# Kernel tuning notes

Measured on AMD Instinct MI355X. Metric: run time of the kernel, lower is better.

Reference implementation:

```python
import jax, jax.numpy as jnp
import numpy as np

B, D, N, K = 8, 3, 65536, 64
EPS = 1e-8

def setup_inputs() -> dict:
    key = jax.random.key(0)
    k1, k2, k3 = jax.random.split(key, 3)
    return {
        "template_features": jax.random.normal(k1, (B, D, N), dtype=jnp.float32),
        "source_features": jax.random.normal(k2, (B, D, N), dtype=jnp.float32),
        "W": jax.random.normal(k3, (D, K), dtype=jnp.float32),
    }

def _gamma(features_t, W):
    # features_t: (B,N,D); logits: (B,K,N); softmax over points (dim=2, as in torch code)
    logits = jnp.einsum('bnd,dk->bkn', features_t, W)
    return jax.nn.softmax(logits, axis=2)

def _gmm_params(gamma, pts):
    # gamma: (B,K,N), pts: (B,N,D)
    n = gamma.shape[2]
    Npi = gamma.sum(axis=2) + EPS                       # (B,K)
    pi = Npi / n
    g = gamma / (Npi[:, :, None] + EPS)                 # (B,K,N)
    mu = jnp.einsum('bkn,bnd->bkd', g, pts)             # weighted mean
    # second moment; exact central form: sum_n g (x-mu)(x-mu)^T = Exx - (2 - s) mu mu^T
    Exx = jnp.einsum('bkn,bnd,bne->bkde', g, pts, pts)
    s = g.sum(axis=2)                                   # (B,K), ~1 (not exactly, due to eps)
    outer = mu[..., :, None] * mu[..., None, :]
    sigma = (Exx - (2.0 - s)[..., None, None] * outer) / (Npi[:, :, None, None] + EPS)
    return pi, mu, sigma

def _estimate_transform(mu_x, pi_x, mu_y, pi_y):
    cx = jnp.sum(mu_x * pi_x[..., None], axis=1, keepdims=True)   # (B,1,D)
    cy = jnp.sum(mu_y * pi_y[..., None], axis=1, keepdims=True)
    mu_x_c = mu_x - cx
    mu_y_c = mu_y - cy
    Wm = jnp.einsum('bkd,bke->bde', pi_x[..., None] * mu_y_c, mu_x_c)  # (B,D,D)
    U, S, Vh = jnp.linalg.svd(Wm, full_matrices=False)
    R = jnp.matmul(U, Vh)
    det = jnp.linalg.det(R)
    Vh = Vh.at[:, :, -1].multiply(jnp.sign(det)[:, None])
    R = jnp.matmul(U, Vh)
    T = cy[:, 0, :] - jnp.einsum('bde,be->bd', R, cx[:, 0, :])
    return R, T

def reference(template_features, source_features, W):
    template_pts = jnp.swapaxes(template_features, 1, 2)   # (B,N,D)
    source_pts = jnp.swapaxes(source_features, 1, 2)
    t_gamma = _gamma(template_pts, W)
    s_gamma = _gamma(source_pts, W)
    t_pi, t_mu, t_sigma = _gmm_params(t_gamma, template_pts)
    s_pi, s_mu, s_sigma = _gmm_params(s_gamma, source_pts)
    R, T = _estimate_transform(s_mu, s_pi, t_mu, t_pi)
    aligned = jnp.matmul(source_pts, jnp.swapaxes(R, 1, 2)) + T[:, None, :]
    return aligned
```

## Files before the change

kernel.cpp:

```cpp
#include <hip/hip_runtime.h>

#define N_PTS 65536
#define BATCH 8
#define KCL   64
#define CHUNK 1024
#define THREADS 256
#define LOG2E 1.44269504088896340736f

__device__ __forceinline__ double drcp(double x) {
    double r = (double)(1.0f / (float)x);
    r = r * (2.0 - x * r);
    r = r * (2.0 - x * r);
    return r;
}

__device__ __forceinline__ float hw_exp2(float x) {
    return __builtin_amdgcn_exp2f(x);
}

__global__ __launch_bounds__(THREADS) void k_sum(const float* __restrict__ tmpl,
                                                 const float* __restrict__ srcf,
                                                 const float* __restrict__ Wmat,
                                                 float* __restrict__ Zs,
                                                 float* __restrict__ Ss) {
    const int chunk = blockIdx.x;
    const int b     = blockIdx.y;
    const int set   = blockIdx.z;
    const float* feat = set ? srcf : tmpl;
    const int n0 = chunk * CHUNK;

    __shared__ float xs[3][CHUNK];
    __shared__ float red[4][KCL][4];

    const int tid = threadIdx.x;
    const float* base = feat + (size_t)b * 3 * N_PTS + n0;
    for (int i = tid; i < 3 * (CHUNK / 4); i += THREADS) {
        int d = i / (CHUNK / 4);
        int p = i % (CHUNK / 4);
        float4 v = ((const float4*)(base + (size_t)d * N_PTS))[p];
        ((float4*)&xs[d][0])[p] = v;
    }
    __syncthreads();

    const int lane = tid & 63;
    const int wv   = tid >> 6;
    const float w0 = Wmat[lane] * LOG2E;
    const float w1 = Wmat[KCL + lane] * LOG2E;
    const float w2 = Wmat[2 * KCL + lane] * LOG2E;

    float z = 0.f, s0 = 0.f, s1 = 0.f, s2 = 0.f;
    const int q0 = wv * (CHUNK / 16);
    for (int q = q0; q < q0 + CHUNK / 16; ++q) {
        float4 a = ((const float4*)&xs[0][0])[q];
        float4 c = ((const float4*)&xs[1][0])[q];
        float4 d = ((const float4*)&xs[2][0])[q];
        {
            float l = fmaf(a.x, w0, fmaf(c.x, w1, d.x * w2));
            float e = hw_exp2(l);
            z += e; s0 = fmaf(e, a.x, s0); s1 = fmaf(e, c.x, s1); s2 = fmaf(e, d.x, s2);
        }
        {
            float l = fmaf(a.y, w0, fmaf(c.y, w1, d.y * w2));
            float e = hw_exp2(l);
            z += e; s0 = fmaf(e, a.y, s0); s1 = fmaf(e, c.y, s1); s2 = fmaf(e, d.y, s2);
        }
        {
            float l = fmaf(a.z, w0, fmaf(c.z, w1, d.z * w2));
            float e = hw_exp2(l);
            z += e; s0 = fmaf(e, a.z, s0); s1 = fmaf(e, c.z, s1); s2 = fmaf(e, d.z, s2);
        }
        {
            float l = fmaf(a.w, w0, fmaf(c.w, w1, d.w * w2));
            float e = hw_exp2(l);
            z += e; s0 = fmaf(e, a.w, s0); s1 = fmaf(e, c.w, s1); s2 = fmaf(e, d.w, s2);
        }
    }
    red[wv][lane][0] = z;
    red[wv][lane][1] = s0;
    red[wv][lane][2] = s1;
    red[wv][lane][3] = s2;
    __syncthreads();
    if (tid < KCL) {
        float rz  = red[0][tid][0] + red[1][tid][0] + red[2][tid][0] + red[3][tid][0];
        float rs0 = red[0][tid][1] + red[1][tid][1] + red[2][tid][1] + red[3][tid][1];
        float rs1 = red[0][tid][2] + red[1][tid][2] + red[2][tid][2] + red[3][tid][2];
        float rs2 = red[0][tid][3] + red[1][tid][3] + red[2][tid][3] + red[3][tid][3];
        int idx = ((int)set * BATCH + b) * KCL + tid;
        atomicAdd(&Zs[idx], rz);
        atomicAdd(&Ss[idx * 3 + 0], rs0);
        atomicAdd(&Ss[idx * 3 + 1], rs1);
        atomicAdd(&Ss[idx * 3 + 2], rs2);
    }
}

__global__ void k_transform(const float* __restrict__ Zs,
                            const float* __restrict__ Ss,
                            float* __restrict__ RT) {
    const int b = threadIdx.x;
    if (b >= BATCH) return;

    const double inv_npi = 1.0 / (1.0 + 2e-8);
    const double pi_c = (1.0 + 1e-8) / (double)N_PTS;

    double Mt[3] = {0, 0, 0}, Ms[3] = {0, 0, 0};
    double P[3][3] = {{0,0,0},{0,0,0},{0,0,0}};
    for (int k = 0; k < KCL; ++k) {
        int it = (0 * BATCH + b) * KCL + k;
        int is = (1 * BATCH + b) * KCL + k;
        double izt = inv_npi * drcp((double)Zs[it]);
        double izs = inv_npi * drcp((double)Zs[is]);
        double mt[3], ms[3];
        for (int d = 0; d < 3; ++d) {
            mt[d] = (double)Ss[it * 3 + d] * izt;
            ms[d] = (double)Ss[is * 3 + d] * izs;
            Mt[d] += mt[d];
            Ms[d] += ms[d];
        }
        for (int d = 0; d < 3; ++d)
            for (int e = 0; e < 3; ++e)
                P[d][e] += mt[d] * ms[e];
    }
    double cy[3], cx[3];
    for (int d = 0; d < 3; ++d) { cy[d] = pi_c * Mt[d]; cx[d] = pi_c * Ms[d]; }

    const double coef = 2.0 * pi_c - 64.0 * pi_c * pi_c;
    double A[3][3];
    for (int d = 0; d < 3; ++d)
        for (int e = 0; e < 3; ++e)
            A[d][e] = pi_c * (P[d][e] - coef * Mt[d] * Ms[e]);

    double G[3][3];
    for (int i = 0; i < 3; ++i)
        for (int j = 0; j < 3; ++j) {
            double acc = 0;
            for (int d = 0; d < 3; ++d) acc += A[d][i] * A[d][j];
            G[i][j] = acc;
        }

    double V[3][3] = {{1,0,0},{0,1,0},{0,0,1}};
    const int pairs[3][2] = {{0,1},{0,2},{1,2}};
    const double scale0 = fabs(G[0][0]) + fabs(G[1][1]) + fabs(G[2][2]) + 1e-300;
    for (int sweep = 0; sweep < 10; ++sweep) {
        double off = fabs(G[0][1]) + fabs(G[0][2]) + fabs(G[1][2]);
        if (off < 1e-28 * scale0) break;
        for (int pi_i = 0; pi_i < 3; ++pi_i) {
            int p = pairs[pi_i][0], q = pairs[pi_i][1];
            double apq = G[p][q];
            if (fabs(apq) < 1e-30 * scale0) continue;
            double tau = (G[q][q] - G[p][p]) * drcp(2.0 * apq);
            double t = ((tau >= 0) ? 1.0 : -1.0) * drcp(fabs(tau) + sqrt(1.0 + tau * tau));
            double c = drcp(sqrt(1.0 + t * t));
            double s = t * c;
            double gpp = G[p][p], gqq = G[q][q];
            G[p][p] = gpp - t * apq;
            G[q][q] = gqq + t * apq;
            G[p][q] = G[q][p] = 0.0;
            int r = 3 - p - q;
            double grp = G[r][p], grq = G[r][q];
            G[r][p] = G[p][r] = c * grp - s * grq;
            G[r][q] = G[q][r] = s * grp + c * grq;
            for (int rr = 0; rr < 3; ++rr) {
                double vrp = V[rr][p], vrq = V[rr][q];
                V[rr][p] = c * vrp - s * vrq;
                V[rr][q] = s * vrp + c * vrq;
            }
        }
    }

    double invs[3];
    for (int i = 0; i < 3; ++i) {
        double lam = G[i][i];
        invs[i] = drcp(sqrt(lam > 1e-300 ? lam : 1e-300));
    }
    double M[3][3];
    for (int i = 0; i < 3; ++i)
        for (int j = 0; j < 3; ++j) {
            double acc = 0;
            for (int m2 = 0; m2 < 3; ++m2) acc += V[i][m2] * V[j][m2] * invs[m2];
            M[i][j] = acc;
        }
    double R0[3][3];
    for (int d = 0; d < 3; ++d)
        for (int e = 0; e < 3; ++e) {
            double acc = 0;
            for (int m2 = 0; m2 < 3; ++m2) acc += A[d][m2] * M[m2][e];
            R0[d][e] = acc;
        }

    double det = R0[0][0] * (R0[1][1] * R0[2][2] - R0[1][2] * R0[2][1])
               - R0[0][1] * (R0[1][0] * R0[2][2] - R0[1][2] * R0[2][0])
               + R0[0][2] * (R0[1][0] * R0[2][1] - R0[1][1] * R0[2][0]);
    double sg = (det >= 0.0) ? 1.0 : -1.0;
    R0[0][2] *= sg; R0[1][2] *= sg; R0[2][2] *= sg;

    double T[3];
    for (int d = 0; d < 3; ++d)
        T[d] = cy[d] - (R0[d][0] * cx[0] + R0[d][1] * cx[1] + R0[d][2] * cx[2]);

    float* rt = RT + b * 12;
    rt[0] = (float)R0[0][0]; rt[1] = (float)R0[0][1]; rt[2] = (float)R0[0][2];
    rt[3] = (float)R0[1][0]; rt[4] = (float)R0[1][1]; rt[5] = (float)R0[1][2];
    rt[6] = (float)R0[2][0]; rt[7] = (float)R0[2][1]; rt[8] = (float)R0[2][2];
    rt[9] = (float)T[0]; rt[10] = (float)T[1]; rt[11] = (float)T[2];
}

__global__ __launch_bounds__(256) void k_apply(const float* __restrict__ srcf,
                                               const float* __restrict__ RT,
                                               float* __restrict__ out) {
    const int idx = blockIdx.x * 256 + threadIdx.x;
    const int b = idx >> 16;
    const int n = idx & (N_PTS - 1);
    const float* rt = RT + b * 12;
    const float* base = srcf + (size_t)b * 3 * N_PTS;
    float x0 = base[n];
    float x1 = base[N_PTS + n];
    float x2 = base[2 * N_PTS + n];
    float y0 = fmaf(rt[0], x0, fmaf(rt[1], x1, fmaf(rt[2], x2, rt[9])));
    float y1 = fmaf(rt[3], x0, fmaf(rt[4], x1, fmaf(rt[5], x2, rt[10])));
    float y2 = fmaf(rt[6], x0, fmaf(rt[7], x1, fmaf(rt[8], x2, rt[11])));
    size_t o = (size_t)idx * 3;
    out[o + 0] = y0;
    out[o + 1] = y1;
    out[o + 2] = y2;
}

extern "C" void kernel_launch(void* const* d_in, const int* in_sizes, int n_in,
                              void* d_out, int out_size, void* d_ws, size_t ws_size,
                              hipStream_t stream) {
    const float* tmpl = (const float*)d_in[0];
    const float* srcf = (const float*)d_in[1];
    const float* Wmat = (const float*)d_in[2];
    float* out = (float*)d_out;

    float* Zs = (float*)d_ws;
    float* Ss = (float*)d_ws + 1024;
    float* RT = (float*)d_ws + 4096;

    (void)hipMemsetAsync(d_ws, 0, 4096 * sizeof(float), stream);

    dim3 grid1(N_PTS / CHUNK, BATCH, 2);
    k_sum<<<grid1, THREADS, 0, stream>>>(tmpl, srcf, Wmat, Zs, Ss);
    k_transform<<<1, 64, 0, stream>>>(Zs, Ss, RT);
    k_apply<<<(BATCH * N_PTS) / 256, 256, 0, stream>>>(srcf, RT, out);
}
```

Baseline: 111.8 us.

## Fuse transform solve into apply kernel and stream inputs directly in k_sum

k_sum no longer stages each chunk through shared memory. Each wave now reads float4 data straight from global memory over a 512-point slice, and the grid is flattened to 512 blocks. The separate single-block k_transform launch is removed. Every k_apply block now recomputes the 3x3 SVD/rotation redundantly in its first wave, using shuffle reductions across 8 lanes per batch, and keeps R/T in shared memory. k_apply also processes 4 points per thread, which cuts one launch and a serial dependency at the cost of duplicated small compute per block.

Result: faster. 100.7 us (-9.9%).

```diff
diff --git a/kernel.cpp b/kernel.cpp
--- a/kernel.cpp
+++ b/kernel.cpp
@@ -3,8 +3,6 @@
 #define N_PTS 65536
 #define BATCH 8
 #define KCL   64
-#define CHUNK 1024
-#define THREADS 256
 #define LOG2E 1.44269504088896340736f
 
 __device__ __forceinline__ double drcp(double x) {
@@ -18,42 +16,34 @@
     return __builtin_amdgcn_exp2f(x);
 }
 
-__global__ __launch_bounds__(THREADS) void k_sum(const float* __restrict__ tmpl,
-                                                 const float* __restrict__ srcf,
-                                                 const float* __restrict__ Wmat,
-                                                 float* __restrict__ Zs,
-                                                 float* __restrict__ Ss) {
-    const int chunk = blockIdx.x;
-    const int b     = blockIdx.y;
-    const int set   = blockIdx.z;
-    const float* feat = set ? srcf : tmpl;
-    const int n0 = chunk * CHUNK;
-
-    __shared__ float xs[3][CHUNK];
-    __shared__ float red[4][KCL][4];
-
-    const int tid = threadIdx.x;
-    const float* base = feat + (size_t)b * 3 * N_PTS + n0;
-    for (int i = tid; i < 3 * (CHUNK / 4); i += THREADS) {
-        int d = i / (CHUNK / 4);
-        int p = i % (CHUNK / 4);
-        float4 v = ((const float4*)(base + (size_t)d * N_PTS))[p];
-        ((float4*)&xs[d][0])[p] = v;
-    }
-    __syncthreads();
-
+__global__ __launch_bounds__(256) void k_sum(const float* __restrict__ tmpl,
+                                             const float* __restrict__ srcf,
+                                             const float* __restrict__ Wmat,
+                                             float* __restrict__ Zs,
+                                             float* __restrict__ Ss) {
+    const int tid  = threadIdx.x;
     const int lane = tid & 63;
     const int wv   = tid >> 6;
+
+    const int gw  = __builtin_amdgcn_readfirstlane(blockIdx.x * 4 + wv);
+    const int set = gw >> 10;
+    const int b   = (gw >> 7) & 7;
+    const int n0  = (gw & 127) * 512;
+    const float* bp = (set ? srcf : tmpl) + (size_t)b * 3 * N_PTS + n0;
+
     const float w0 = Wmat[lane] * LOG2E;
     const float w1 = Wmat[KCL + lane] * LOG2E;
     const float w2 = Wmat[2 * KCL + lane] * LOG2E;
 
     float z = 0.f, s0 = 0.f, s1 = 0.f, s2 = 0.f;
-    const int q0 = wv * (CHUNK / 16);
-    for (int q = q0; q < q0 + CHUNK / 16; ++q) {
-        float4 a = ((const float4*)&xs[0][0])[q];
-        float4 c = ((const float4*)&xs[1][0])[q];
-        float4 d = ((const float4*)&xs[2][0])[q];
+    const float4* p0 = (const float4*)bp;
+    const float4* p1 = (const float4*)(bp + N_PTS);
+    const float4* p2 = (const float4*)(bp + 2 * N_PTS);
+#pragma unroll 4
+    for (int q = 0; q < 128; ++q) {
+        float4 a = p0[q];
+        float4 c = p1[q];
+        float4 d = p2[q];
         {
             float l = fmaf(a.x, w0, fmaf(c.x, w1, d.x * w2));
             float e = hw_exp2(l);
@@ -75,6 +65,8 @@
             z += e; s0 = fmaf(e, a.w, s0); s1 = fmaf(e, c.w, s1); s2 = fmaf(e, d.w, s2);
         }
     }
+
+    __shared__ float red[4][KCL][4];
     red[wv][lane][0] = z;
     red[wv][lane][1] = s0;
     red[wv][lane][2] = s1;
@@ -85,7 +77,7 @@
         float rs0 = red[0][tid][1] + red[1][tid][1] + red[2][tid][1] + red[3][tid][1];
         float rs1 = red[0][tid][2] + red[1][tid][2] + red[2][tid][2] + red[3][tid][2];
         float rs2 = red[0][tid][3] + red[1][tid][3] + red[2][tid][3] + red[3][tid][3];
-        int idx = ((int)set * BATCH + b) * KCL + tid;
+        int idx = (set * BATCH + b) * KCL + tid;
         atomicAdd(&Zs[idx], rz);
         atomicAdd(&Ss[idx * 3 + 0], rs0);
         atomicAdd(&Ss[idx * 3 + 1], rs1);
@@ -93,135 +85,154 @@
     }
 }
 
-__global__ void k_transform(const float* __restrict__ Zs,
-                            const float* __restrict__ Ss,
-                            float* __restrict__ RT) {
-    const int b = threadIdx.x;
-    if (b >= BATCH) return;
-
-    const double inv_npi = 1.0 / (1.0 + 2e-8);
-    const double pi_c = (1.0 + 1e-8) / (double)N_PTS;
-
-    double Mt[3] = {0, 0, 0}, Ms[3] = {0, 0, 0};
-    double P[3][3] = {{0,0,0},{0,0,0},{0,0,0}};
-    for (int k = 0; k < KCL; ++k) {
-        int it = (0 * BATCH + b) * KCL + k;
-        int is = (1 * BATCH + b) * KCL + k;
-        double izt = inv_npi * drcp((double)Zs[it]);
-        double izs = inv_npi * drcp((double)Zs[is]);
-        double mt[3], ms[3];
-        for (int d = 0; d < 3; ++d) {
-            mt[d] = (double)Ss[it * 3 + d] * izt;
-            ms[d] = (double)Ss[is * 3 + d] * izs;
-            Mt[d] += mt[d];
-            Ms[d] += ms[d];
-        }
+__global__ __launch_bounds__(256) void k_apply(const float* __restrict__ srcf,
+                                               const float* __restrict__ Zs,
+                                               const float* __restrict__ Ss,
+                                               float* __restrict__ out) {
+    __shared__ float rt_s[BATCH][12];
+
+    if (threadIdx.x < 64) {
+        const int lane = threadIdx.x;
+        const int b    = lane >> 3;
+        const int sub  = lane & 7;
+
+        const double inv_npi = 1.0 / (1.0 + 2e-8);
+        const double pi_c = (1.0 + 1e-8) / (double)N_PTS;
+
+        double Mt[3] = {0, 0, 0}, Ms[3] = {0, 0, 0};
+        double P[3][3] = {{0,0,0},{0,0,0},{0,0,0}};
+        for (int kk = 0; kk < 8; ++kk) {
+            int k  = sub * 8 + kk;
+            int it = b * KCL + k;
+            int is = (BATCH + b) * KCL + k;
+            double izt = inv_npi * drcp((double)Zs[it]);
+            double izs = inv_npi * drcp((double)Zs[is]);
+            double mt[3], ms[3];
+            for (int d = 0; d < 3; ++d) {
+                mt[d] = (double)Ss[it * 3 + d] * izt;
+                ms[d] = (double)Ss[is * 3 + d] * izs;
+                Mt[d] += mt[d];
+                Ms[d] += ms[d];
+            }
+            for (int d = 0; d < 3; ++d)
+                for (int e = 0; e < 3; ++e)
+                    P[d][e] += mt[d] * ms[e];
+        }
+        for (int m = 1; m <= 4; m <<= 1) {
+            for (int d = 0; d < 3; ++d) {
+                Mt[d] += __shfl_xor(Mt[d], m, 64);
+                Ms[d] += __shfl_xor(Ms[d], m, 64);
+            }
+            for (int d = 0; d < 3; ++d)
+                for (int e = 0; e < 3; ++e)
+                    P[d][e] += __shfl_xor(P[d][e], m, 64);
+        }
+
+        double cy[3], cx[3];
+        for (int d = 0; d < 3; ++d) { cy[d] = pi_c * Mt[d]; cx[d] = pi_c * Ms[d]; }
+
+        const double coef = 2.0 * pi_c - 64.0 * pi_c * pi_c;
+        double A[3][3];
         for (int d = 0; d < 3; ++d)
             for (int e = 0; e < 3; ++e)
-                P[d][e] += mt[d] * ms[e];
-    }
-    double cy[3], cx[3];
-    for (int d = 0; d < 3; ++d) { cy[d] = pi_c * Mt[d]; cx[d] = pi_c * Ms[d]; }
-
-    const double coef = 2.0 * pi_c - 64.0 * pi_c * pi_c;
-    double A[3][3];
-    for (int d = 0; d < 3; ++d)
-        for (int e = 0; e < 3; ++e)
-            A[d][e] = pi_c * (P[d][e] - coef * Mt[d] * Ms[e]);
-
-    double G[3][3];
-    for (int i = 0; i < 3; ++i)
-        for (int j = 0; j < 3; ++j) {
-            double acc = 0;
-            for (int d = 0; d < 3; ++d) acc += A[d][i] * A[d][j];
-            G[i][j] = acc;
-        }
-
-    double V[3][3] = {{1,0,0},{0,1,0},{0,0,1}};
-    const int pairs[3][2] = {{0,1},{0,2},{1,2}};
-    const double scale0 = fabs(G[0][0]) + fabs(G[1][1]) + fabs(G[2][2]) + 1e-300;
-    for (int sweep = 0; sweep < 10; ++sweep) {
-        double off = fabs(G[0][1]) + fabs(G[0][2]) + fabs(G[1][2]);
-        if (off < 1e-28 * scale0) break;
-        for (int pi_i = 0; pi_i < 3; ++pi_i) {
-            int p = pairs[pi_i][0], q = pairs[pi_i][1];
-            double apq = G[p][q];
-            if (fabs(apq) < 1e-30 * scale0) continue;
-            double tau = (G[q][q] - G[p][p]) * drcp(2.0 * apq);
-            double t = ((tau >= 0) ? 1.0 : -1.0) * drcp(fabs(tau) + sqrt(1.0 + tau * tau));
-            double c = drcp(sqrt(1.0 + t * t));
-            double s = t * c;
-            double gpp = G[p][p], gqq = G[q][q];
-            G[p][p] = gpp - t * apq;
-            G[q][q] = gqq + t * apq;
-            G[p][q] = G[q][p] = 0.0;
-            int r = 3 - p - q;
-            double grp = G[r][p], grq = G[r][q];
-            G[r][p] = G[p][r] = c * grp - s * grq;
-            G[r][q] = G[q][r] = s * grp + c * grq;
-            for (int rr = 0; rr < 3; ++rr) {
-                double vrp = V[rr][p], vrq = V[rr][q];
-                V[rr][p] = c * vrp - s * vrq;
-                V[rr][q] = s * vrp + c * vrq;
-            }
-        }
-    }
-
-    double invs[3];
-    for (int i = 0; i < 3; ++i) {
-        double lam = G[i][i];
-        invs[i] = drcp(sqrt(lam > 1e-300 ? lam : 1e-300));
-    }
-    double M[3][3];
-    for (int i = 0; i < 3; ++i)
-        for (int j = 0; j < 3; ++j) {
-            double acc = 0;
-            for (int m2 = 0; m2 < 3; ++m2) acc += V[i][m2] * V[j][m2] * invs[m2];
-            M[i][j] = acc;
-        }
-    double R0[3][3];
-    for (int d = 0; d < 3; ++d)
-        for (int e = 0; e < 3; ++e) {
-            double acc = 0;
-            for (int m2 = 0; m2 < 3; ++m2) acc += A[d][m2] * M[m2][e];
-            R0[d][e] = acc;
-        }
-
-    double det = R0[0][0] * (R0[1][1] * R0[2][2] - R0[1][2] * R0[2][1])
-               - R0[0][1] * (R0[1][0] * R0[2][2] - R0[1][2] * R0[2][0])
-               + R0[0][2] * (R0[1][0] * R0[2][1] - R0[1][1] * R0[2][0]);
-    double sg = (det >= 0.0) ? 1.0 : -1.0;
-    R0[0][2] *= sg; R0[1][2] *= sg; R0[2][2] *= sg;
-
-    double T[3];
-    for (int d = 0; d < 3; ++d)
-        T[d] = cy[d] - (R0[d][0] * cx[0] + R0[d][1] * cx[1] + R0[d][2] * cx[2]);
-
-    float* rt = RT + b * 12;
-    rt[0] = (float)R0[0][0]; rt[1] = (float)R0[0][1]; rt[2] = (float)R0[0][2];
-    rt[3] = (float)R0[1][0]; rt[4] = (float)R0[1][1]; rt[5] = (float)R0[1][2];
-    rt[6] = (float)R0[2][0]; rt[7] = (float)R0[2][1]; rt[8] = (float)R0[2][2];
-    rt[9] = (float)T[0]; rt[10] = (float)T[1]; rt[11] = (float)T[2];
-}
-
-__global__ __launch_bounds__(256) void k_apply(const float* __restrict__ srcf,
-                                               const float* __restrict__ RT,
-                                               float* __restrict__ out) {
-    const int idx = blockIdx.x * 256 + threadIdx.x;
-    const int b = idx >> 16;
-    const int n = idx & (N_PTS - 1);
-    const float* rt = RT + b * 12;
-    const float* base = srcf + (size_t)b * 3 * N_PTS;
-    float x0 = base[n];
-    float x1 = base[N_PTS + n];
-    float x2 = base[2 * N_PTS + n];
-    float y0 = fmaf(rt[0], x0, fmaf(rt[1], x1, fmaf(rt[2], x2, rt[9])));
-    float y1 = fmaf(rt[3], x0, fmaf(rt[4], x1, fmaf(rt[5], x2, rt[10])));
-    float y2 = fmaf(rt[6], x0, fmaf(rt[7], x1, fmaf(rt[8], x2, rt[11])));
-    size_t o = (size_t)idx * 3;
-    out[o + 0] = y0;
-    out[o + 1] = y1;
-    out[o + 2] = y2;
+                A[d][e] = pi_c * (P[d][e] - coef * Mt[d] * Ms[e]);
+
+        double G[3][3];
+        for (int i = 0; i < 3; ++i)
+            for (int j = 0; j < 3; ++j) {
+                double acc = 0;
+                for (int d = 0; d < 3; ++d) acc += A[d][i] * A[d][j];
+                G[i][j] = acc;
+            }
+
+        double V[3][3] = {{1,0,0},{0,1,0},{0,0,1}};
+        const int pairs[3][2] = {{0,1},{0,2},{1,2}};
+        const double scale0 = fabs(G[0][0]) + fabs(G[1][1]) + fabs(G[2][2]) + 1e-300;
+        for (int sweep = 0; sweep < 10; ++sweep) {
+            double off = fabs(G[0][1]) + fabs(G[0][2]) + fabs(G[1][2]);
+            if (off < 1e-28 * scale0) break;
+            for (int pi_i = 0; pi_i < 3; ++pi_i) {
+                int p = pairs[pi_i][0], q = pairs[pi_i][1];
+                double apq = G[p][q];
+                if (fabs(apq) < 1e-30 * scale0) continue;
+                double tau = (G[q][q] - G[p][p]) * drcp(2.0 * apq);
+                double t = ((tau >= 0) ? 1.0 : -1.0) * drcp(fabs(tau) + sqrt(1.0 + tau * tau));
+                double c = drcp(sqrt(1.0 + t * t));
+                double s = t * c;
+                double gpp = G[p][p], gqq = G[q][q];
+                G[p][p] = gpp - t * apq;
+                G[q][q] = gqq + t * apq;
+                G[p][q] = G[q][p] = 0.0;
+                int r = 3 - p - q;
+                double grp = G[r][p], grq = G[r][q];
+                G[r][p] = G[p][r] = c * grp - s * grq;
+                G[r][q] = G[q][r] = s * grp + c * grq;
+                for (int rr = 0; rr < 3; ++rr) {
+                    double vrp = V[rr][p], vrq = V[rr][q];
+                    V[rr][p] = c * vrp - s * vrq;
+                    V[rr][q] = s * vrp + c * vrq;
+                }
+            }
+        }
+
+        double invs[3];
+        for (int i = 0; i < 3; ++i) {
+            double lam = G[i][i];
+            invs[i] = drcp(sqrt(lam > 1e-300 ? lam : 1e-300));
+        }
+        double M[3][3];
+        for (int i = 0; i < 3; ++i)
+            for (int j = 0; j < 3; ++j) {
+                double acc = 0;
+                for (int m2 = 0; m2 < 3; ++m2) acc += V[i][m2] * V[j][m2] * invs[m2];
+                M[i][j] = acc;
+            }
+        double R0[3][3];
+        for (int d = 0; d < 3; ++d)
+            for (int e = 0; e < 3; ++e) {
+                double acc = 0;
+                for (int m2 = 0; m2 < 3; ++m2) acc += A[d][m2] * M[m2][e];
+                R0[d][e] = acc;
+            }
+
+        double det = R0[0][0] * (R0[1][1] * R0[2][2] - R0[1][2] * R0[2][1])
+                   - R0[0][1] * (R0[1][0] * R0[2][2] - R0[1][2] * R0[2][0])
+                   + R0[0][2] * (R0[1][0] * R0[2][1] - R0[1][1] * R0[2][0]);
+        double sg = (det >= 0.0) ? 1.0 : -1.0;
+        R0[0][2] *= sg; R0[1][2] *= sg; R0[2][2] *= sg;
+
+        double T[3];
+        for (int d = 0; d < 3; ++d)
+            T[d] = cy[d] - (R0[d][0] * cx[0] + R0[d][1] * cx[1] + R0[d][2] * cx[2]);
+
+        if (sub == 0) {
+            rt_s[b][0] = (float)R0[0][0]; rt_s[b][1] = (float)R0[0][1]; rt_s[b][2] = (float)R0[0][2];
+            rt_s[b][3] = (float)R0[1][0]; rt_s[b][4] = (float)R0[1][1]; rt_s[b][5] = (float)R0[1][2];
+            rt_s[b][6] = (float)R0[2][0]; rt_s[b][7] = (float)R0[2][1]; rt_s[b][8] = (float)R0[2][2];
+            rt_s[b][9] = (float)T[0]; rt_s[b][10] = (float)T[1]; rt_s[b][11] = (float)T[2];
+        }
+    }
+    __syncthreads();
+
+    const int t = blockIdx.x * 256 + threadIdx.x;
+#pragma unroll
+    for (int i = 0; i < 4; ++i) {
+        int idx = t + i * 131072;
+        int b = idx >> 16;
+        int n = idx & (N_PTS - 1);
+        const float* rt = rt_s[b];
+        const float* base = srcf + (size_t)b * 3 * N_PTS;
+        float x0 = base[n];
+        float x1 = base[N_PTS + n];
+        float x2 = base[2 * N_PTS + n];
+        float y0 = fmaf(rt[0], x0, fmaf(rt[1], x1, fmaf(rt[2], x2, rt[9])));
+        float y1 = fmaf(rt[3], x0, fmaf(rt[4], x1, fmaf(rt[5], x2, rt[10])));
+        float y2 = fmaf(rt[6], x0, fmaf(rt[7], x1, fmaf(rt[8], x2, rt[11])));
+        size_t o = (size_t)idx * 3;
+        out[o + 0] = y0;
+        out[o + 1] = y1;
+        out[o + 2] = y2;
+    }
 }
 
 extern "C" void kernel_launch(void* const* d_in, const int* in_sizes, int n_in,
@@ -234,12 +245,9 @@
 
     float* Zs = (float*)d_ws;
     float* Ss = (float*)d_ws + 1024;
-    float* RT = (float*)d_ws + 4096;
 
     (void)hipMemsetAsync(d_ws, 0, 4096 * sizeof(float), stream);
 
-    dim3 grid1(N_PTS / CHUNK, BATCH, 2);
-    k_sum<<<grid1, THREADS, 0, stream>>>(tmpl, srcf, Wmat, Zs, Ss);
-    k_transform<<<1, 64, 0, stream>>>(Zs, Ss, RT);
-    k_apply<<<(BATCH * N_PTS) / 256, 256, 0, stream>>>(srcf, RT, out);
-}
+    k_sum<<<512, 256, 0, stream>>>(tmpl, srcf, Wmat, Zs, Ss);
+    k_apply<<<512, 256, 0, stream>>>(srcf, Zs, Ss, out);
+}
```
